# Kernel optimization log

Measured on AMD Instinct MI355X. Metric: run time of the kernel, lower is better.

The kernel has to match this reference:

```python
import jax, jax.numpy as jnp
import numpy as np

B, S, D = 4, 1024, 1024
H, HD = 16, 64  # num_heads, head_dim; H*HD == D (qkv_features)
NEG_BIG = -1e10


def setup_inputs() -> dict:
    key = jax.random.key(0)
    ks = jax.random.split(key, 16)
    inp = {
        'inputs_q': jax.random.normal(ks[0], (B, S, D), jnp.float32),
        'inputs_kv': jax.random.normal(ks[1], (B, S, D), jnp.float32),
        'pos_emb_q': jax.random.normal(ks[2], (B, S, D), jnp.float32),
        'pos_emb_k': jax.random.normal(ks[3], (B, S, D), jnp.float32),
        'pos_emb_v': jax.random.normal(ks[4], (B, S, D), jnp.float32),
        'key_padding_mask': jnp.ones((B, S), jnp.float32),
    }
    scale = 1.0 / np.sqrt(D)
    inp['wq'] = jax.random.normal(ks[5], (D, H, HD), jnp.float32) * scale
    inp['bq'] = jnp.zeros((H, HD), jnp.float32)
    inp['wk'] = jax.random.normal(ks[6], (D, H, HD), jnp.float32) * scale
    inp['bk'] = jnp.zeros((H, HD), jnp.float32)
    inp['wv'] = jax.random.normal(ks[7], (D, H, HD), jnp.float32) * scale
    inp['bv'] = jnp.zeros((H, HD), jnp.float32)
    inp['wo'] = jax.random.normal(ks[8], (H, HD, D), jnp.float32) * scale
    inp['bo'] = jnp.zeros((D,), jnp.float32)
    return inp


def reference(inputs_q, inputs_kv, pos_emb_q, pos_emb_k, pos_emb_v,
              key_padding_mask, wq, bq, wk, bk, wv, bv, wo, bo):
    # Add positional embeddings before QKV projections (DETR style).
    q_in = inputs_q + pos_emb_q
    k_in = inputs_kv + pos_emb_k
    v_in = inputs_kv + pos_emb_v
    # DenseGeneral: [b,s,f] x [f,h,d] -> [b,s,h,d]
    q = jnp.einsum('bsf,fhd->bshd', q_in, wq) + bq
    k = jnp.einsum('bsf,fhd->bshd', k_in, wk) + bk
    v = jnp.einsum('bsf,fhd->bshd', v_in, wv) + bv
    # Additive key-padding bias, broadcast to [b,1,1,kv].
    bias = ((1.0 - key_padding_mask) * NEG_BIG)[:, None, None, :]
    q = q / jnp.sqrt(jnp.asarray(HD, q.dtype))
    attn = jnp.einsum('bqhd,bkhd->bhqk', q, k) + bias
    attn = jax.nn.softmax(attn, axis=-1)
    # (train=False: no dropout; identity capture layer is a no-op.)
    x = jnp.einsum('bhqk,bkhd->bqhd', attn, v)
    # Output projection over (heads, head_dim).
    out = jnp.einsum('bqhd,hdf->bqf', x, wo) + bo
    return out
```

## Files before the change

kernel.cpp:

```cpp
#include <hip/hip_runtime.h>
#include <hip/hip_bf16.h>
#include <stdint.h>

typedef __bf16 bf16_t;
typedef __bf16 bf16x8 __attribute__((ext_vector_type(8)));
typedef __bf16 bf16x4v __attribute__((ext_vector_type(4)));
typedef float  f32x4  __attribute__((ext_vector_type(4)));
typedef float  f32x16 __attribute__((ext_vector_type(16)));
typedef unsigned int u32;
typedef u32 u32x4 __attribute__((ext_vector_type(4)));

#define NEG_BIG (-1e10f)
#define LOG2E 1.44269504f

__device__ __forceinline__ void load_lds16(const void* gsrc, void* ldst) {
  __builtin_amdgcn_global_load_lds(
      (__attribute__((address_space(1))) void*)(gsrc),
      (__attribute__((address_space(3))) void*)(ldst), 16, 0, 0);
}

__device__ __forceinline__ u32 cvt_pk_bf16(float lo, float hi) {
  u32 r;
  asm("v_cvt_pk_bf16_f32 %0, %1, %2" : "=v"(r) : "v"(lo), "v"(hi));
  return r;
}

__global__ __launch_bounds__(256) void k_prep_w(
    const float* __restrict__ iq, const float* __restrict__ ikv,
    const float* __restrict__ pq, const float* __restrict__ pk, const float* __restrict__ pv,
    const float* __restrict__ wq, const float* __restrict__ wk,
    const float* __restrict__ wv, const float* __restrict__ wo,
    bf16_t* __restrict__ Xq, bf16_t* __restrict__ Xk, bf16_t* __restrict__ Xv,
    bf16_t* __restrict__ Wt, bf16_t* __restrict__ Wot)
{
  __shared__ float t[64][65];
  if (blockIdx.x < 2048) {
    size_t t0 = (size_t)blockIdx.x * 256 + threadIdx.x;
    size_t f4 = t0 * 2;
    float4 a0 = ((const float4*)iq)[f4],  a1 = ((const float4*)iq)[f4+1];
    float4 b0 = ((const float4*)ikv)[f4], b1 = ((const float4*)ikv)[f4+1];
    float4 eq0 = ((const float4*)pq)[f4], eq1 = ((const float4*)pq)[f4+1];
    float4 ek0 = ((const float4*)pk)[f4], ek1 = ((const float4*)pk)[f4+1];
    float4 ev0 = ((const float4*)pv)[f4], ev1 = ((const float4*)pv)[f4+1];
    bf16x8 q, k, v;
    q[0]=(bf16_t)(a0.x+eq0.x); q[1]=(bf16_t)(a0.y+eq0.y); q[2]=(bf16_t)(a0.z+eq0.z); q[3]=(bf16_t)(a0.w+eq0.w);
    q[4]=(bf16_t)(a1.x+eq1.x); q[5]=(bf16_t)(a1.y+eq1.y); q[6]=(bf16_t)(a1.z+eq1.z); q[7]=(bf16_t)(a1.w+eq1.w);
    k[0]=(bf16_t)(b0.x+ek0.x); k[1]=(bf16_t)(b0.y+ek0.y); k[2]=(bf16_t)(b0.z+ek0.z); k[3]=(bf16_t)(b0.w+ek0.w);
    k[4]=(bf16_t)(b1.x+ek1.x); k[5]=(bf16_t)(b1.y+ek1.y); k[6]=(bf16_t)(b1.z+ek1.z); k[7]=(bf16_t)(b1.w+ek1.w);
    v[0]=(bf16_t)(b0.x+ev0.x); v[1]=(bf16_t)(b0.y+ev0.y); v[2]=(bf16_t)(b0.z+ev0.z); v[3]=(bf16_t)(b0.w+ev0.w);
    v[4]=(bf16_t)(b1.x+ev1.x); v[5]=(bf16_t)(b1.y+ev1.y); v[6]=(bf16_t)(b1.z+ev1.z); v[7]=(bf16_t)(b1.w+ev1.w);
    *(bf16x8*)&Xq[t0*8] = q;
    *(bf16x8*)&Xk[t0*8] = k;
    *(bf16x8*)&Xv[t0*8] = v;
  } else {
    int bid = blockIdx.x - 2048;
    int z = bid >> 8, rem = bid & 255;
    const float* src = z==0 ? wq : z==1 ? wk : z==2 ? wv : wo;
    bf16_t*      dst = z < 3 ? (Wt + (size_t)z*(1u<<20)) : Wot;
    int n0 = (rem & 15) << 6, k0 = (rem >> 4) << 6;
    int c = threadIdx.x & 63, rb = threadIdx.x >> 6;
    #pragma unroll
    for (int i = 0; i < 16; ++i) {
      int r = i*4 + rb;
      t[r][c] = src[(size_t)(k0 + r)*1024 + n0 + c];
    }
    __syncthreads();
    int n = threadIdx.x & 63, hq = threadIdx.x >> 6;
    #pragma unroll
    for (int j = 0; j < 2; ++j) {
      int kk = hq*2 + j;
      bf16x8 vv;
      #pragma unroll
      for (int e = 0; e < 8; ++e) vv[e] = (bf16_t)t[kk*8 + e][n];
      *(bf16x8*)&dst[(size_t)(n0 + n)*1024 + k0 + kk*8] = vv;
    }
  }
}

__global__ __launch_bounds__(256, 3) void k_gemm_qkv(
    const bf16_t* __restrict__ Xq, const bf16_t* __restrict__ Xk, const bf16_t* __restrict__ Xv,
    const bf16_t* __restrict__ Wt,
    const float* __restrict__ bq, const float* __restrict__ bk, const float* __restrict__ bv,
    bf16_t* __restrict__ Qo, bf16_t* __restrict__ Ko, bf16_t* __restrict__ Vt)
{
  const int L = blockIdx.x;
  const int w = (L & 7) * 96 + (L >> 3);
  const int bx = w & 7, by = (w >> 3) & 31, bz = w >> 8;
  const int bn = bz * 8 + bx;

  const bf16_t* A = bz==0 ? Xq : bz==1 ? Xk : Xv;
  const float* bias = bz==0 ? bq : bz==1 ? bk : bv;

  __shared__ bf16_t As[128*64];
  __shared__ bf16_t Bs[128*64];

  const int tid = threadIdx.x, lane = tid & 63, wid = tid >> 6;
  const int wm = wid >> 1, wn = wid & 1;
  const int bm0 = by * 128;
  const int bn0g = bn * 128;
  const int g = lane >> 4, c = lane & 15;
  const int sr = lane >> 3, sch = lane & 7;

  f32x4 acc[4][4] = {};

  #define STAGE(kt_)                                                             \
    { _Pragma("unroll")                                                          \
      for (int i = 0; i < 4; ++i) {                                              \
        int r  = wid*32 + i*8 + sr;                                              \
        int ca = sch ^ (r & 7);                                                  \
        load_lds16(A  + (size_t)(bm0  + r)*1024 + (size_t)(kt_)*64 + ca*8,       \
                   &As[(wid*32 + i*8)*64]);                                      \
        load_lds16(Wt + (size_t)(bn0g + r)*1024 + (size_t)(kt_)*64 + ca*8,       \
                   &Bs[(wid*32 + i*8)*64]);                                      \
      } }

  for (int kt = 0; kt < 16; ++kt) {
    STAGE(kt);
    __syncthreads();
    #pragma unroll
    for (int kk = 0; kk < 2; ++kk) {
      bf16x8 af[4], bfr[4];
      #pragma unroll
      for (int m = 0; m < 4; ++m) {
        int row = wm*64 + m*16 + c;
        int ch  = (kk*4 + g) ^ (row & 7);
        af[m] = *(const bf16x8*)&As[row*64 + ch*8];
      }
      #pragma unroll
      for (int n = 0; n < 4; ++n) {
        int row = wn*64 + n*16 + c;
        int ch  = (kk*4 + g) ^ (row & 7);
        bfr[n] = *(const bf16x8*)&Bs[row*64 + ch*8];
      }
      #pragma unroll
      for (int m = 0; m < 4; ++m)
        #pragma unroll
        for (int n = 0; n < 4; ++n)
          acc[m][n] = __builtin_amdgcn_mfma_f32_16x16x32_bf16(af[m], bfr[n], acc[m][n], 0, 0, 0);
    }
    __syncthreads();
  }
  #undef STAGE

  if (bz < 2) {
    bf16_t* C = bz==0 ? Qo : Ko;
    const float scale = bz==0 ? 0.125f * LOG2E : 1.0f;
    #pragma unroll
    for (int n = 0; n < 4; ++n) {
      int col = (bn0g & 1023) + wn*64 + n*16 + c;
      float bn_ = bias[col];
      #pragma unroll
      for (int m = 0; m < 4; ++m) {
        int row0 = bm0 + wm*64 + m*16 + g*4;
        #pragma unroll
        for (int r = 0; r < 4; ++r)
          C[(size_t)(row0 + r)*1024 + col] = (bf16_t)((acc[m][n][r] + bn_) * scale);
      }
    }
  } else {
    #pragma unroll
    for (int n = 0; n < 4; ++n) {
      int colz = (bn0g & 1023) + wn*64 + n*16 + c;
      float bn_ = bias[colz];
      int h = colz >> 6, hd = colz & 63;
      #pragma unroll
      for (int m = 0; m < 4; ++m) {
        int row0 = bm0 + wm*64 + m*16 + g*4;
        int b = row0 >> 10, s0 = row0 & 1023;
        bf16x4v v4;
        #pragma unroll
        for (int r = 0; r < 4; ++r) v4[r] = (bf16_t)(acc[m][n][r] + bn_);
        *(bf16x4v*)&Vt[(size_t)((b*16 + h)*64 + hd)*1024 + s0] = v4;
      }
    }
  }
}

__global__ __launch_bounds__(512, 4) void k_attn2(
    const bf16_t* __restrict__ Qm, const bf16_t* __restrict__ Km,
    const bf16_t* __restrict__ Vt, const float* __restrict__ mask,
    bf16_t* __restrict__ X2)
{
  __shared__ bf16_t Ks[2][2][64*64];
  __shared__ bf16_t Vs[2][2][64*64];
  __shared__ float  bias_lds[1024];
  __shared__ int    tflag[16];
  __shared__ float  l_lds[4][32];
  __shared__ float  l2_lds[4][32];

  const int L = blockIdx.x;
  const int kk_ = L >> 3;
  const int bh = (L & 7) * 8 + (kk_ >> 3);
  const int qt = kk_ & 7;
  const int b = bh >> 4, h = bh & 15;

  const int tid = threadIdx.x, lane = tid & 63, wid = tid >> 6;
  const int half = wid >> 2, w4 = wid & 3;
  const int lq = lane & 31;
  const int hi = lane >> 5;

  if (tid < 16) tflag[tid] = 0;
  __syncthreads();
  {
    float2 m2 = *(const float2*)&mask[b*1024 + tid*2];
    float2 b2;
    b2.x = (1.0f - m2.x) * (NEG_BIG * LOG2E);
    b2.y = (1.0f - m2.y) * (NEG_BIG * LOG2E);
    *(float2*)&bias_lds[tid*2] = b2;
    if (b2.x != 0.f || b2.y != 0.f)
      tflag[tid >> 5] = 1;
  }

  const int q0w = qt*128 + w4*32;
  bf16x8 qf[4];
  #pragma unroll
  for (int kb = 0; kb < 4; ++kb)
    qf[kb] = *(const bf16x8*)&Qm[(size_t)(b*1024 + q0w + lq)*1024 + h*64 + kb*16 + hi*8];

  f32x16 oacc[2] = {};
  float lsum = 0.f;

  const int sr8 = (lane >> 3);
  const int sc8 = lane & 7;
  #define STAGE(bufi, kv0)                                                        \
    {                                                                             \
      _Pragma("unroll")                                                           \
      for (int cc = 0; cc < 2; ++cc) {                                            \
        int r  = cc*32 + w4*8 + sr8;                                              \
        int ca = sc8 ^ (r & 7);                                                   \
        load_lds16(Km + (size_t)(b*1024 + (kv0) + r)*1024 + h*64 + ca*8,          \
                   &Ks[half][bufi][(cc*32 + w4*8)*64]);                           \
        load_lds16(Vt + (size_t)((b*16 + h)*64 + r)*1024 + (kv0) + ca*8,          \
                   &Vs[half][bufi][(cc*32 + w4*8)*64]);                           \
      }                                                                           \
    }

  STAGE(0, half*512);
  __syncthreads();

  for (int t = 0; t < 8; ++t) {
    const int kt = half*8 + t;
    const int buf = t & 1;
    if (t < 7) STAGE(buf ^ 1, (kt + 1) * 64);

    f32x16 s[2];
    __builtin_amdgcn_s_setprio(1);
    #pragma unroll
    for (int blk = 0; blk < 2; ++blk) {
      f32x16 acc = {};
      #pragma unroll
      for (int kb = 0; kb < 4; ++kb) {
        int row = blk*32 + lq;
        int ch  = (kb*2 + hi) ^ (row & 7);
        bf16x8 kf = *(const bf16x8*)&Ks[half][buf][row*64 + ch*8];
        acc = __builtin_amdgcn_mfma_f32_32x32x16_bf16(kf, qf[kb], acc, 0, 0, 0);
      }
      s[blk] = acc;
    }
    __builtin_amdgcn_s_setprio(0);

    if (tflag[kt]) {
      #pragma unroll
      for (int blk = 0; blk < 2; ++blk)
        #pragma unroll
        for (int g2 = 0; g2 < 4; ++g2) {
          float4 b4 = *(const float4*)&bias_lds[kt*64 + blk*32 + g2*8 + hi*4];
          s[blk][g2*4+0] += b4.x;
          s[blk][g2*4+1] += b4.y;
          s[blk][g2*4+2] += b4.z;
          s[blk][g2*4+3] += b4.w;
        }
    }

    #pragma unroll
    for (int blk = 0; blk < 2; ++blk)
      #pragma unroll
      for (int r = 0; r < 16; ++r) {
        float sv = fminf(s[blk][r], 60.0f);
        asm("v_exp_f32 %0, %1" : "=v"(sv) : "v"(sv));
        s[blk][r] = sv;
      }

    float ts[8];
    #pragma unroll
    for (int r = 0; r < 8; ++r)
      ts[r] = (s[0][r] + s[0][r+8]) + (s[1][r] + s[1][r+8]);
    float s0 = (ts[0] + ts[1]) + (ts[2] + ts[3]);
    float s1 = (ts[4] + ts[5]) + (ts[6] + ts[7]);
    float rsum = s0 + s1;
    lsum += rsum + __shfl_xor(rsum, 32, 64);

    u32 paw[4][4];
    #pragma unroll
    for (int blk = 0; blk < 2; ++blk)
      #pragma unroll
      for (int hf = 0; hf < 2; ++hf) {
        int base = hf * 8;
        #pragma unroll
        for (int w2 = 0; w2 < 2; ++w2) {
          u32 x = cvt_pk_bf16(s[blk][base + 2*w2],     s[blk][base + 2*w2 + 1]);
          u32 y = cvt_pk_bf16(s[blk][base + 4 + 2*w2], s[blk][base + 4 + 2*w2 + 1]);
          asm("v_permlane32_swap_b32 %0, %1" : "+v"(x), "+v"(y));
          paw[blk*2 + hf][w2]     = x;
          paw[blk*2 + hf][w2 + 2] = y;
        }
      }

    __builtin_amdgcn_s_setprio(1);
    #pragma unroll
    for (int ks = 0; ks < 4; ++ks) {
      u32x4 t2 = { paw[ks][0], paw[ks][1], paw[ks][2], paw[ks][3] };
      bf16x8 pa = __builtin_bit_cast(bf16x8, t2);
      #pragma unroll
      for (int nb = 0; nb < 2; ++nb) {
        int row = nb*32 + lq;
        int ch  = (ks*2 + hi) ^ (row & 7);
        bf16x8 vf = *(const bf16x8*)&Vs[half][buf][row*64 + ch*8];
        oacc[nb] = __builtin_amdgcn_mfma_f32_32x32x16_bf16(pa, vf, oacc[nb], 0, 0, 0);
      }
    }
    __builtin_amdgcn_s_setprio(0);
    __syncthreads();
  }
  #undef STAGE

  float* obuf = (float*)&Vs[0][0][0];
  if (half == 1) {
    l2_lds[w4][lq] = lsum;
    #pragma unroll
    for (int nb = 0; nb < 2; ++nb)
      #pragma unroll
      for (int reg = 0; reg < 16; ++reg)
        obuf[((((w4*2 + hi)*16 + reg)*2) + nb)*32 + lq] = oacc[nb][reg];
  }
  __syncthreads();
  if (half == 0) {
    float lt = lsum + l2_lds[w4][lq];
    l_lds[w4][lq] = lt;
  }
  __syncthreads();
  if (half == 0) {
    #pragma unroll
    for (int g2 = 0; g2 < 4; ++g2)
      #pragma unroll
      for (int j = 0; j < 4; ++j) {
        int reg  = g2*4 + j;
        int qrow = j + 8*g2 + 4*hi;
        float inv = 1.0f / l_lds[w4][qrow];
        #pragma unroll
        for (int nb = 0; nb < 2; ++nb) {
          float o = oacc[nb][reg] + obuf[((((w4*2 + hi)*16 + reg)*2) + nb)*32 + lq];
          X2[(size_t)(b*1024 + q0w + qrow)*1024 + h*64 + nb*32 + lq] = (bf16_t)(o * inv);
        }
      }
  }
}

__global__ __launch_bounds__(256, 3) void k_gemm_out(
    const bf16_t* __restrict__ A, const bf16_t* __restrict__ Bt,
    const float* __restrict__ bo, float* __restrict__ C)
{
  const int L = blockIdx.x;
  const int w = (L & 7) * 32 + (L >> 3);
  const int bx = w & 7, by = w >> 3;

  __shared__ bf16_t As[128*64];
  __shared__ bf16_t Bs[128*64];

  const int tid = threadIdx.x, lane = tid & 63, wid = tid >> 6;
  const int wm = wid >> 1, wn = wid & 1;
  const int bm0 = by * 128, bn0 = bx * 128;
  const int g = lane >> 4, c = lane & 15;
  const int sr = lane >> 3, sch = lane & 7;

  f32x4 acc[4][4] = {};

  #define STAGEO(kt_)                                                            \
    { _Pragma("unroll")                                                          \
      for (int i = 0; i < 4; ++i) {                                              \
        int r  = wid*32 + i*8 + sr;                                              \
        int ca = sch ^ (r & 7);                                                  \
        load_lds16(A  + (size_t)(bm0 + r)*1024 + (size_t)(kt_)*64 + ca*8,        \
                   &As[(wid*32 + i*8)*64]);                                      \
        load_lds16(Bt + (size_t)(bn0 + r)*1024 + (size_t)(kt_)*64 + ca*8,        \
                   &Bs[(wid*32 + i*8)*64]);                                      \
      } }

  for (int kt = 0; kt < 16; ++kt) {
    STAGEO(kt);
    __syncthreads();
    #pragma unroll
    for (int kk = 0; kk < 2; ++kk) {
      bf16x8 af[4], bfr[4];
      #pragma unroll
      for (int m = 0; m < 4; ++m) {
        int row = wm*64 + m*16 + c;
        int ch  = (kk*4 + g) ^ (row & 7);
        af[m] = *(const bf16x8*)&As[row*64 + ch*8];
      }
      #pragma unroll
      for (int n = 0; n < 4; ++n) {
        int row = wn*64 + n*16 + c;
        int ch  = (kk*4 + g) ^ (row & 7);
        bfr[n] = *(const bf16x8*)&Bs[row*64 + ch*8];
      }
      #pragma unroll
      for (int m = 0; m < 4; ++m)
        #pragma unroll
        for (int n = 0; n < 4; ++n)
          acc[m][n] = __builtin_amdgcn_mfma_f32_16x16x32_bf16(af[m], bfr[n], acc[m][n], 0, 0, 0);
    }
    __syncthreads();
  }
  #undef STAGEO

  #pragma unroll
  for (int n = 0; n < 4; ++n) {
    int col = bn0 + wn*64 + n*16 + c;
    float bn_ = bo[col];
    #pragma unroll
    for (int m = 0; m < 4; ++m) {
      int row0 = bm0 + wm*64 + m*16 + g*4;
      #pragma unroll
      for (int r = 0; r < 4; ++r)
        C[(size_t)(row0 + r)*1024 + col] = acc[m][n][r] + bn_;
    }
  }
}

extern "C" void kernel_launch(void* const* d_in, const int* in_sizes, int n_in,
                              void* d_out, int out_size, void* d_ws, size_t ws_size,
                              hipStream_t stream) {
  const float* iq   = (const float*)d_in[0];
  const float* ikv  = (const float*)d_in[1];
  const float* pq   = (const float*)d_in[2];
  const float* pk   = (const float*)d_in[3];
  const float* pv   = (const float*)d_in[4];
  const float* mask = (const float*)d_in[5];
  const float* wq   = (const float*)d_in[6];
  const float* bq   = (const float*)d_in[7];
  const float* wk   = (const float*)d_in[8];
  const float* bk   = (const float*)d_in[9];
  const float* wv   = (const float*)d_in[10];
  const float* bv   = (const float*)d_in[11];
  const float* wo   = (const float*)d_in[12];
  const float* bo   = (const float*)d_in[13];
  float* out = (float*)d_out;

  char* ws = (char*)d_ws;
  bf16_t* Xq  = (bf16_t*)(ws + (size_t)( 0u<<20));
  bf16_t* Xk  = (bf16_t*)(ws + (size_t)( 8u<<20));
  bf16_t* Xv  = (bf16_t*)(ws + (size_t)(16u<<20));
  bf16_t* Wt  = (bf16_t*)(ws + (size_t)(24u<<20));
  bf16_t* Wot = (bf16_t*)(ws + (size_t)(30u<<20));
  bf16_t* Q   = (bf16_t*)(ws + (size_t)(32u<<20));
  bf16_t* K   = (bf16_t*)(ws + (size_t)(40u<<20));
  bf16_t* Vt  = (bf16_t*)(ws + (size_t)(56u<<20));
  bf16_t* X2  = (bf16_t*)(ws + (size_t)(64u<<20));

  k_prep_w<<<3072, 256, 0, stream>>>(iq, ikv, pq, pk, pv, wq, wk, wv, wo,
                                     Xq, Xk, Xv, Wt, Wot);
  k_gemm_qkv<<<768, 256, 0, stream>>>(Xq, Xk, Xv, Wt, bq, bk, bv, Q, K, Vt);
  k_attn2<<<512, 512, 0, stream>>>(Q, K, Vt, mask, X2);
  k_gemm_out<<<256, 256, 0, stream>>>(X2, Wot, bo, out);
}
```

Baseline: 107.9 us.

## Fuse positional-embedding add and bf16 cast into QKV GEMM A-tile load

```diff
diff --git a/kernel.cpp b/kernel.cpp
--- a/kernel.cpp
+++ b/kernel.cpp
@@ -25,60 +25,38 @@
   return r;
 }
 
-__global__ __launch_bounds__(256) void k_prep_w(
-    const float* __restrict__ iq, const float* __restrict__ ikv,
-    const float* __restrict__ pq, const float* __restrict__ pk, const float* __restrict__ pv,
+__global__ __launch_bounds__(256) void k_wtrans(
     const float* __restrict__ wq, const float* __restrict__ wk,
     const float* __restrict__ wv, const float* __restrict__ wo,
-    bf16_t* __restrict__ Xq, bf16_t* __restrict__ Xk, bf16_t* __restrict__ Xv,
     bf16_t* __restrict__ Wt, bf16_t* __restrict__ Wot)
 {
   __shared__ float t[64][65];
-  if (blockIdx.x < 2048) {
-    size_t t0 = (size_t)blockIdx.x * 256 + threadIdx.x;
-    size_t f4 = t0 * 2;
-    float4 a0 = ((const float4*)iq)[f4],  a1 = ((const float4*)iq)[f4+1];
-    float4 b0 = ((const float4*)ikv)[f4], b1 = ((const float4*)ikv)[f4+1];
-    float4 eq0 = ((const float4*)pq)[f4], eq1 = ((const float4*)pq)[f4+1];
-    float4 ek0 = ((const float4*)pk)[f4], ek1 = ((const float4*)pk)[f4+1];
-    float4 ev0 = ((const float4*)pv)[f4], ev1 = ((const float4*)pv)[f4+1];
-    bf16x8 q, k, v;
-    q[0]=(bf16_t)(a0.x+eq0.x); q[1]=(bf16_t)(a0.y+eq0.y); q[2]=(bf16_t)(a0.z+eq0.z); q[3]=(bf16_t)(a0.w+eq0.w);
-    q[4]=(bf16_t)(a1.x+eq1.x); q[5]=(bf16_t)(a1.y+eq1.y); q[6]=(bf16_t)(a1.z+eq1.z); q[7]=(bf16_t)(a1.w+eq1.w);
-    k[0]=(bf16_t)(b0.x+ek0.x); k[1]=(bf16_t)(b0.y+ek0.y); k[2]=(bf16_t)(b0.z+ek0.z); k[3]=(bf16_t)(b0.w+ek0.w);
-    k[4]=(bf16_t)(b1.x+ek1.x); k[5]=(bf16_t)(b1.y+ek1.y); k[6]=(bf16_t)(b1.z+ek1.z); k[7]=(bf16_t)(b1.w+ek1.w);
-    v[0]=(bf16_t)(b0.x+ev0.x); v[1]=(bf16_t)(b0.y+ev0.y); v[2]=(bf16_t)(b0.z+ev0.z); v[3]=(bf16_t)(b0.w+ev0.w);
-    v[4]=(bf16_t)(b1.x+ev1.x); v[5]=(bf16_t)(b1.y+ev1.y); v[6]=(bf16_t)(b1.z+ev1.z); v[7]=(bf16_t)(b1.w+ev1.w);
-    *(bf16x8*)&Xq[t0*8] = q;
-    *(bf16x8*)&Xk[t0*8] = k;
-    *(bf16x8*)&Xv[t0*8] = v;
-  } else {
-    int bid = blockIdx.x - 2048;
-    int z = bid >> 8, rem = bid & 255;
-    const float* src = z==0 ? wq : z==1 ? wk : z==2 ? wv : wo;
-    bf16_t*      dst = z < 3 ? (Wt + (size_t)z*(1u<<20)) : Wot;
-    int n0 = (rem & 15) << 6, k0 = (rem >> 4) << 6;
-    int c = threadIdx.x & 63, rb = threadIdx.x >> 6;
-    #pragma unroll
-    for (int i = 0; i < 16; ++i) {
-      int r = i*4 + rb;
-      t[r][c] = src[(size_t)(k0 + r)*1024 + n0 + c];
-    }
-    __syncthreads();
-    int n = threadIdx.x & 63, hq = threadIdx.x >> 6;
-    #pragma unroll
-    for (int j = 0; j < 2; ++j) {
-      int kk = hq*2 + j;
-      bf16x8 vv;
-      #pragma unroll
-      for (int e = 0; e < 8; ++e) vv[e] = (bf16_t)t[kk*8 + e][n];
-      *(bf16x8*)&dst[(size_t)(n0 + n)*1024 + k0 + kk*8] = vv;
-    }
-  }
-}
-
-__global__ __launch_bounds__(256, 3) void k_gemm_qkv(
-    const bf16_t* __restrict__ Xq, const bf16_t* __restrict__ Xk, const bf16_t* __restrict__ Xv,
+  int bid = blockIdx.x;
+  int z = bid >> 8, rem = bid & 255;
+  const float* src = z==0 ? wq : z==1 ? wk : z==2 ? wv : wo;
+  bf16_t*      dst = z < 3 ? (Wt + (size_t)z*(1u<<20)) : Wot;
+  int n0 = (rem & 15) << 6, k0 = (rem >> 4) << 6;
+  int c = threadIdx.x & 63, rb = threadIdx.x >> 6;
+  #pragma unroll
+  for (int i = 0; i < 16; ++i) {
+    int r = i*4 + rb;
+    t[r][c] = src[(size_t)(k0 + r)*1024 + n0 + c];
+  }
+  __syncthreads();
+  int n = threadIdx.x & 63, hq = threadIdx.x >> 6;
+  #pragma unroll
+  for (int j = 0; j < 2; ++j) {
+    int kk = hq*2 + j;
+    bf16x8 vv;
+    #pragma unroll
+    for (int e = 0; e < 8; ++e) vv[e] = (bf16_t)t[kk*8 + e][n];
+    *(bf16x8*)&dst[(size_t)(n0 + n)*1024 + k0 + kk*8] = vv;
+  }
+}
+
+__global__ __launch_bounds__(256, 2) void k_gemm_qkv(
+    const float* __restrict__ iq, const float* __restrict__ ikv,
+    const float* __restrict__ pq, const float* __restrict__ pk, const float* __restrict__ pv,
     const bf16_t* __restrict__ Wt,
     const float* __restrict__ bq, const float* __restrict__ bk, const float* __restrict__ bv,
     bf16_t* __restrict__ Qo, bf16_t* __restrict__ Ko, bf16_t* __restrict__ Vt)
@@ -88,7 +66,8 @@
   const int bx = w & 7, by = (w >> 3) & 31, bz = w >> 8;
   const int bn = bz * 8 + bx;
 
-  const bf16_t* A = bz==0 ? Xq : bz==1 ? Xk : Xv;
+  const float* Ain = bz==0 ? iq : ikv;
+  const float* Pin = bz==0 ? pq : (bz==1 ? pk : pv);
   const float* bias = bz==0 ? bq : bz==1 ? bk : bv;
 
   __shared__ bf16_t As[128*64];
@@ -103,19 +82,28 @@
 
   f32x4 acc[4][4] = {};
 
-  #define STAGE(kt_)                                                             \
-    { _Pragma("unroll")                                                          \
-      for (int i = 0; i < 4; ++i) {                                              \
-        int r  = wid*32 + i*8 + sr;                                              \
-        int ca = sch ^ (r & 7);                                                  \
-        load_lds16(A  + (size_t)(bm0  + r)*1024 + (size_t)(kt_)*64 + ca*8,       \
-                   &As[(wid*32 + i*8)*64]);                                      \
-        load_lds16(Wt + (size_t)(bn0g + r)*1024 + (size_t)(kt_)*64 + ca*8,       \
-                   &Bs[(wid*32 + i*8)*64]);                                      \
-      } }
-
   for (int kt = 0; kt < 16; ++kt) {
-    STAGE(kt);
+    const int kc0 = kt * 64;
+    #pragma unroll
+    for (int i = 0; i < 4; ++i) {
+      int r  = wid*32 + i*8 + sr;
+      int ca = sch ^ (r & 7);
+      load_lds16(Wt + (size_t)(bn0g + r)*1024 + kc0 + ca*8, &Bs[(wid*32 + i*8)*64]);
+    }
+    #pragma unroll
+    for (int j = 0; j < 4; ++j) {
+      int r = wid*32 + j*8 + sr;
+      size_t off = (size_t)(bm0 + r)*1024 + kc0 + sch*8;
+      f32x4 a0 = *(const f32x4*)&Ain[off], a1 = *(const f32x4*)&Ain[off + 4];
+      f32x4 p0 = *(const f32x4*)&Pin[off], p1 = *(const f32x4*)&Pin[off + 4];
+      bf16x8 vv;
+      #pragma unroll
+      for (int e = 0; e < 4; ++e) {
+        vv[e]     = (bf16_t)(a0[e] + p0[e]);
+        vv[e + 4] = (bf16_t)(a1[e] + p1[e]);
+      }
+      *(bf16x8*)&As[r*64 + (sch ^ (r & 7))*8] = vv;
+    }
     __syncthreads();
     #pragma unroll
     for (int kk = 0; kk < 2; ++kk) {
@@ -140,7 +128,6 @@
     }
     __syncthreads();
   }
-  #undef STAGE
 
   if (bz < 2) {
     bf16_t* C = bz==0 ? Qo : Ko;
@@ -448,9 +435,6 @@
   float* out = (float*)d_out;
 
   char* ws = (char*)d_ws;
-  bf16_t* Xq  = (bf16_t*)(ws + (size_t)( 0u<<20));
-  bf16_t* Xk  = (bf16_t*)(ws + (size_t)( 8u<<20));
-  bf16_t* Xv  = (bf16_t*)(ws + (size_t)(16u<<20));
   bf16_t* Wt  = (bf16_t*)(ws + (size_t)(24u<<20));
   bf16_t* Wot = (bf16_t*)(ws + (size_t)(30u<<20));
   bf16_t* Q   = (bf16_t*)(ws + (size_t)(32u<<20));
@@ -458,9 +442,8 @@
   bf16_t* Vt  = (bf16_t*)(ws + (size_t)(56u<<20));
   bf16_t* X2  = (bf16_t*)(ws + (size_t)(64u<<20));
 
-  k_prep_w<<<3072, 256, 0, stream>>>(iq, ikv, pq, pk, pv, wq, wk, wv, wo,
-                                     Xq, Xk, Xv, Wt, Wot);
-  k_gemm_qkv<<<768, 256, 0, stream>>>(Xq, Xk, Xv, Wt, bq, bk, bv, Q, K, Vt);
+  k_wtrans<<<1024, 256, 0, stream>>>(wq, wk, wv, wo, Wt, Wot);
+  k_gemm_qkv<<<768, 256, 0, stream>>>(iq, ikv, pq, pk, pv, Wt, bq, bk, bv, Q, K, Vt);
   k_attn2<<<512, 512, 0, stream>>>(Q, K, Vt, mask, X2);
   k_gemm_out<<<256, 256, 0, stream>>>(X2, Wot, bo, out);
 }
```

Measured after the change: 137.0 us. 1.27x slower.
